# Optimization experiments

Hardware: AMD Instinct MI355X
Metric: run time of the kernel (lower is better)

Reference implementation:

```python
import jax, jax.numpy as jnp
import numpy as np

N = 2_000_000  # number of 3x3 SPD matrices (DTI-scale volume)


def _make_spd(key, n):
    # M M^T + 0.5 I is symmetric positive definite with generically distinct eigenvalues
    m = jax.random.normal(key, (n, 3, 3), dtype=jnp.float32)
    return m @ jnp.swapaxes(m, -1, -2) + 0.5 * jnp.eye(3, dtype=jnp.float32)


def setup_inputs() -> dict:
    key = jax.random.key(0)
    k1, k2 = jax.random.split(key)
    return {"D1": _make_spd(k1, N), "D2": _make_spd(k2, N)}


def _logm_spd(D):
    # Batched symmetric matrix log via eigendecomposition: V diag(log w) V^T
    w, v = jnp.linalg.eigh(D)                    # w: [N,3], v: [N,3,3]
    return (v * jnp.log(w)[..., None, :]) @ jnp.swapaxes(v, -1, -2)


def reference(D1, D2):
    # Log-Euclidean SPD distance: ||logm(D1) - logm(D2)||_F, then mean of squares
    diff = _logm_spd(D1) - _logm_spd(D2)         # [N,3,3]
    sq_dist = jnp.sum(diff * diff, axis=(-1, -2))  # [N]
    return jnp.mean(sq_dist)
```

## Files before the change

### kernel.cpp

```cpp
#include <hip/hip_runtime.h>
#include <hip/hip_bf16.h>

#define BLOCK 256
#define TILE 256

__device__ __forceinline__ float frcp(float x) { return __builtin_amdgcn_rcpf(x); }
__device__ __forceinline__ float fsqrt(float x) { return __builtin_amdgcn_sqrtf(x); }

__device__ __forceinline__ float facos(float x) {
    float ax = fabsf(x);
    float sq = fsqrt(fmaxf(1.0f - ax, 0.0f));
    float poly = fmaf(fmaf(fmaf(-0.0187293f, ax, 0.0742610f), ax, -0.2121144f),
                      ax, 1.5707288f);
    float ac = sq * poly;
    return (x < 0.0f) ? (3.14159274f - ac) : ac;
}

__device__ __forceinline__ void logm3(const float m[6], float L[6]) {
    float a00 = m[0], a01 = m[1], a02 = m[2];
    float a11 = m[3], a12 = m[4], a22 = m[5];

    float q  = (a00 + a11 + a22) * (1.0f / 3.0f);
    float b00 = a00 - q, b11 = a11 - q, b22 = a22 - q;
    float p2 = b00*b00 + b11*b11 + b22*b22
             + 2.0f * (a01*a01 + a02*a02 + a12*a12);
    float p  = fsqrt(p2 * (1.0f / 6.0f));
    p = fmaxf(p, 1e-12f);
    float ip = frcp(p);
    float c00 = b00*ip, c11 = b11*ip, c22 = b22*ip;
    float c01 = a01*ip, c02 = a02*ip, c12 = a12*ip;
    float detB = c00*(c11*c22 - c12*c12)
               - c01*(c01*c22 - c12*c02)
               + c02*(c01*c12 - c11*c02);
    float r = fminf(fmaxf(0.5f * detB, -1.0f), 1.0f);
    float phi = facos(r) * (1.0f / 3.0f);
    float sph = __sinf(phi), cph = __cosf(phi);
    float whi = q + 2.0f * p * cph;
    float wlo = q - p * (cph + 1.7320508f * sph);
    float wmid = 3.0f * q - whi - wlo;
    float w0 = fmaxf(wlo,  1e-8f);
    float w1 = fmaxf(wmid, 1e-8f);
    float w2 = fmaxf(whi,  1e-8f);

    float l0 = __logf(w0), l1 = __logf(w1), l2 = __logf(w2);
    float d01 = w1 - w0, d12 = w2 - w1, span = w2 - w0;
    float thr = 1e-3f * w1;
    float dd01 = (d01 > thr) ? (l1 - l0) * frcp(d01) : 2.0f * frcp(w0 + w1);
    float dd12 = (d12 > thr) ? (l2 - l1) * frcp(d12) : 2.0f * frcp(w1 + w2);
    float dd012 = (span > thr) ? (dd12 - dd01) * frcp(span)
                               : -0.5f * frcp(w1 * w1);
    float k2 = dd012;
    float k1 = dd01 - dd012 * (w0 + w1);
    float k0 = l0 - dd01 * w0 + dd012 * (w0 * w1);

    float s00 = a00*a00 + a01*a01 + a02*a02;
    float s01 = a00*a01 + a01*a11 + a02*a12;
    float s02 = a00*a02 + a01*a12 + a02*a22;
    float s11 = a01*a01 + a11*a11 + a12*a12;
    float s12 = a01*a02 + a11*a12 + a12*a22;
    float s22 = a02*a02 + a12*a12 + a22*a22;

    L[0] = k0 + k1*a00 + k2*s00;
    L[1] =      k1*a01 + k2*s01;
    L[2] =      k1*a02 + k2*s02;
    L[3] = k0 + k1*a11 + k2*s11;
    L[4] =      k1*a12 + k2*s12;
    L[5] = k0 + k1*a22 + k2*s22;
}

__device__ __forceinline__ void load6(const float* a, float m[6]) {
    m[0] = a[0]; m[1] = a[1]; m[2] = a[2];
    m[3] = a[4]; m[4] = a[5]; m[5] = a[8];
}

__device__ __forceinline__ float fnorm2_diff(const float L1[6], const float L2[6]) {
    float d0 = L1[0]-L2[0], d1 = L1[1]-L2[1], d2 = L1[2]-L2[2];
    float d3 = L1[3]-L2[3], d4 = L1[4]-L2[4], d5 = L1[5]-L2[5];
    return d0*d0 + d3*d3 + d5*d5 + 2.0f * (d1*d1 + d2*d2 + d4*d4);
}

__device__ __forceinline__ void load_tile(float2 v[9],
                                          const float* __restrict__ D1,
                                          const float* __restrict__ D2,
                                          long tile, int tid) {
    const float2* s1 = reinterpret_cast<const float2*>(D1 + tile * (TILE * 9));
    const float2* s2 = reinterpret_cast<const float2*>(D2 + tile * (TILE * 9));
    #pragma unroll
    for (int k = 0; k < 9; ++k) {
        int idx = k * BLOCK + tid;
        v[k] = (idx < TILE * 9 / 2) ? s1[idx] : s2[idx - TILE * 9 / 2];
    }
}

__global__ void __launch_bounds__(BLOCK)
le_partial(const float* __restrict__ D1, const float* __restrict__ D2,
           float* __restrict__ partial, int n) {
    __shared__ float lds[TILE * 18];
    __shared__ float wsum[BLOCK / 64];
    float2* lds2 = reinterpret_cast<float2*>(lds);
    const int tid = threadIdx.x;
    const int nfull = n / TILE;
    float acc = 0.0f;

    float2 v[9];
    long t = blockIdx.x;
    if (t < nfull) load_tile(v, D1, D2, t, tid);

    while (t < nfull) {
        __syncthreads();
        #pragma unroll
        for (int k = 0; k < 9; ++k) lds2[k * BLOCK + tid] = v[k];
        long tn = t + gridDim.x;
        if (tn < nfull) load_tile(v, D1, D2, tn, tid);
        __syncthreads();

        float m1[6], m2[6], L1[6], L2[6];
        load6(&lds[tid * 9], m1);
        load6(&lds[TILE * 9 + tid * 9], m2);
        logm3(m1, L1);
        logm3(m2, L2);
        acc += fnorm2_diff(L1, L2);
        t = tn;
    }

    {
        int ti = nfull * TILE + blockIdx.x * BLOCK + tid;
        if (ti < n) {
            float m1[6], m2[6], L1[6], L2[6];
            load6(D1 + (size_t)ti * 9, m1);
            load6(D2 + (size_t)ti * 9, m2);
            logm3(m1, L1);
            logm3(m2, L2);
            acc += fnorm2_diff(L1, L2);
        }
    }

    #pragma unroll
    for (int off = 32; off > 0; off >>= 1)
        acc += __shfl_down(acc, off, 64);
    if ((tid & 63) == 0) wsum[tid >> 6] = acc;
    __syncthreads();
    if (tid == 0) {
        float s = 0.0f;
        #pragma unroll
        for (int i = 0; i < BLOCK / 64; ++i) s += wsum[i];
        partial[blockIdx.x] = s;
    }
}

__global__ void __launch_bounds__(BLOCK)
le_final(const float* __restrict__ partial, int nparts,
         float* __restrict__ out, double invN) {
    double s = 0.0;
    for (int i = threadIdx.x; i < nparts; i += BLOCK)
        s += (double)partial[i];
    #pragma unroll
    for (int off = 32; off > 0; off >>= 1)
        s += __shfl_down(s, off, 64);
    __shared__ double ws[BLOCK / 64];
    if ((threadIdx.x & 63) == 0) ws[threadIdx.x >> 6] = s;
    __syncthreads();
    if (threadIdx.x == 0) {
        double t = 0.0;
        #pragma unroll
        for (int i = 0; i < BLOCK / 64; ++i) t += ws[i];
        out[0] = (float)(t * invN);
    }
}

extern "C" void kernel_launch(void* const* d_in, const int* in_sizes, int n_in,
                              void* d_out, int out_size, void* d_ws, size_t ws_size,
                              hipStream_t stream) {
    const float* D1 = (const float*)d_in[0];
    const float* D2 = (const float*)d_in[1];
    float* out = (float*)d_out;
    float* partial = (float*)d_ws;

    int n = in_sizes[0] / 9;
    int nfull = n / TILE;

    int grid = nfull < 2048 ? (nfull < 1 ? 1 : nfull) : 2048;
    int maxblocks = (int)(ws_size / sizeof(float));
    if (maxblocks > 0 && grid > maxblocks) grid = maxblocks;
    if (grid < 1) grid = 1;

    le_partial<<<grid, BLOCK, 0, stream>>>(D1, D2, partial, n);
    le_final<<<1, BLOCK, 0, stream>>>(partial, grid, out, 1.0 / (double)n);
}
```

Before: 33.24 us.

## Replace LDS-staged tile loads with direct per-thread strided loads and register prefetch

Removes the shared-memory tile staging and its two barriers per iteration. Each thread now loads its own six upper-triangular entries straight from global memory in a grid-stride loop, prefetching the next element into registers. The determinant is computed on the unscaled shifted matrix and scaled by the cubed reciprocal once, which saves multiplies. The trade-off is strided, non-vectorized global access (36-byte stride) instead of coalesced float2 loads, which depends on cache reuse.

```diff
diff --git a/kernel.cpp b/kernel.cpp
--- a/kernel.cpp
+++ b/kernel.cpp
@@ -2,7 +2,6 @@
 #include <hip/hip_bf16.h>
 
 #define BLOCK 256
-#define TILE 256
 
 __device__ __forceinline__ float frcp(float x) { return __builtin_amdgcn_rcpf(x); }
 __device__ __forceinline__ float fsqrt(float x) { return __builtin_amdgcn_sqrtf(x); }
@@ -27,12 +26,11 @@
     float p  = fsqrt(p2 * (1.0f / 6.0f));
     p = fmaxf(p, 1e-12f);
     float ip = frcp(p);
-    float c00 = b00*ip, c11 = b11*ip, c22 = b22*ip;
-    float c01 = a01*ip, c02 = a02*ip, c12 = a12*ip;
-    float detB = c00*(c11*c22 - c12*c12)
-               - c01*(c01*c22 - c12*c02)
-               + c02*(c01*c12 - c11*c02);
-    float r = fminf(fmaxf(0.5f * detB, -1.0f), 1.0f);
+    float detB = b00*(b11*b22 - a12*a12)
+               - a01*(a01*b22 - a12*a02)
+               + a02*(a01*a12 - b11*a02);
+    float ip3 = ip * ip * ip;
+    float r = fminf(fmaxf(0.5f * detB * ip3, -1.0f), 1.0f);
     float phi = facos(r) * (1.0f / 3.0f);
     float sph = __sinf(phi), cph = __cosf(phi);
     float whi = q + 2.0f * p * cph;
@@ -68,7 +66,7 @@
     L[5] = k0 + k1*a22 + k2*s22;
 }
 
-__device__ __forceinline__ void load6(const float* a, float m[6]) {
+__device__ __forceinline__ void load6(const float* __restrict__ a, float m[6]) {
     m[0] = a[0]; m[1] = a[1]; m[2] = a[2];
     m[3] = a[4]; m[4] = a[5]; m[5] = a[8];
 }
@@ -79,71 +77,45 @@
     return d0*d0 + d3*d3 + d5*d5 + 2.0f * (d1*d1 + d2*d2 + d4*d4);
 }
 
-__device__ __forceinline__ void load_tile(float2 v[9],
-                                          const float* __restrict__ D1,
-                                          const float* __restrict__ D2,
-                                          long tile, int tid) {
-    const float2* s1 = reinterpret_cast<const float2*>(D1 + tile * (TILE * 9));
-    const float2* s2 = reinterpret_cast<const float2*>(D2 + tile * (TILE * 9));
-    #pragma unroll
-    for (int k = 0; k < 9; ++k) {
-        int idx = k * BLOCK + tid;
-        v[k] = (idx < TILE * 9 / 2) ? s1[idx] : s2[idx - TILE * 9 / 2];
-    }
-}
-
 __global__ void __launch_bounds__(BLOCK)
 le_partial(const float* __restrict__ D1, const float* __restrict__ D2,
            float* __restrict__ partial, int n) {
-    __shared__ float lds[TILE * 18];
-    __shared__ float wsum[BLOCK / 64];
-    float2* lds2 = reinterpret_cast<float2*>(lds);
     const int tid = threadIdx.x;
-    const int nfull = n / TILE;
+    const long stride = (long)gridDim.x * BLOCK;
+    long i = (long)blockIdx.x * BLOCK + tid;
     float acc = 0.0f;
 
-    float2 v[9];
-    long t = blockIdx.x;
-    if (t < nfull) load_tile(v, D1, D2, t, tid);
+    float m1[6], m2[6];
+    bool have = (i < n);
+    if (have) { load6(D1 + i * 9, m1); load6(D2 + i * 9, m2); }
 
-    while (t < nfull) {
-        __syncthreads();
-        #pragma unroll
-        for (int k = 0; k < 9; ++k) lds2[k * BLOCK + tid] = v[k];
-        long tn = t + gridDim.x;
-        if (tn < nfull) load_tile(v, D1, D2, tn, tid);
-        __syncthreads();
+    while (have) {
+        long inext = i + stride;
+        bool hn = (inext < n);
+        float n1[6], n2[6];
+        if (hn) { load6(D1 + inext * 9, n1); load6(D2 + inext * 9, n2); }
 
-        float m1[6], m2[6], L1[6], L2[6];
-        load6(&lds[tid * 9], m1);
-        load6(&lds[TILE * 9 + tid * 9], m2);
+        float L1[6], L2[6];
         logm3(m1, L1);
         logm3(m2, L2);
         acc += fnorm2_diff(L1, L2);
-        t = tn;
-    }
 
-    {
-        int ti = nfull * TILE + blockIdx.x * BLOCK + tid;
-        if (ti < n) {
-            float m1[6], m2[6], L1[6], L2[6];
-            load6(D1 + (size_t)ti * 9, m1);
-            load6(D2 + (size_t)ti * 9, m2);
-            logm3(m1, L1);
-            logm3(m2, L2);
-            acc += fnorm2_diff(L1, L2);
-        }
+        #pragma unroll
+        for (int k = 0; k < 6; ++k) { m1[k] = n1[k]; m2[k] = n2[k]; }
+        i = inext;
+        have = hn;
     }
 
     #pragma unroll
     for (int off = 32; off > 0; off >>= 1)
         acc += __shfl_down(acc, off, 64);
+    __shared__ float wsum[BLOCK / 64];
     if ((tid & 63) == 0) wsum[tid >> 6] = acc;
     __syncthreads();
     if (tid == 0) {
         float s = 0.0f;
         #pragma unroll
-        for (int i = 0; i < BLOCK / 64; ++i) s += wsum[i];
+        for (int i2 = 0; i2 < BLOCK / 64; ++i2) s += wsum[i2];
         partial[blockIdx.x] = s;
     }
 }
@@ -177,9 +149,9 @@
     float* partial = (float*)d_ws;
 
     int n = in_sizes[0] / 9;
-    int nfull = n / TILE;
+    int nblk = (n + BLOCK - 1) / BLOCK;
 
-    int grid = nfull < 2048 ? (nfull < 1 ? 1 : nfull) : 2048;
+    int grid = nblk < 2048 ? nblk : 2048;
     int maxblocks = (int)(ws_size / sizeof(float));
     if (maxblocks > 0 && grid > maxblocks) grid = maxblocks;
     if (grid < 1) grid = 1;
```

Result: no change. 33.01 us (-0.7%).
